# Optimization experiments

Measured on AMD Instinct MI355X. Metric: run time of the kernel, lower is better.

The kernel has to match this reference:

```python
import jax, jax.numpy as jnp
import numpy as np

N, E = 40000, 640000
DIN, HID, H = 512, 128, 4
C = HID  # per-head channels; H*C == 512 == DIN
BN_EPS = 1e-5


def setup_inputs() -> dict:
    key = jax.random.key(0)
    ks = jax.random.split(key, 32)
    sc = 0.05
    d = {}
    d["x"] = jax.random.normal(ks[0], (N, DIN), jnp.float32)
    d["edge_index"] = jax.random.randint(ks[1], (2, E), 0, N)
    i = 2
    for l in (1, 2, 3):
        d[f"W{l}"] = jax.random.normal(ks[i], (DIN, H * C), jnp.float32) * sc; i += 1
        d[f"as{l}"] = jax.random.normal(ks[i], (H, C), jnp.float32) * sc; i += 1
        d[f"ad{l}"] = jax.random.normal(ks[i], (H, C), jnp.float32) * sc; i += 1
        d[f"b{l}"] = jnp.zeros((H * C,), jnp.float32)
        d[f"g{l}"] = jnp.ones((H * C,), jnp.float32)
        d[f"be{l}"] = jnp.zeros((H * C,), jnp.float32)
    d["Wg1"] = jax.random.normal(ks[i], (H * C, HID), jnp.float32) * sc; i += 1
    d["bg1"] = jnp.zeros((HID,), jnp.float32)
    d["Wg2"] = jax.random.normal(ks[i], (HID, 1), jnp.float32) * sc; i += 1
    d["bg2"] = jnp.zeros((1,), jnp.float32)
    d["Wf1"] = jax.random.normal(ks[i], (H * C, HID), jnp.float32) * sc; i += 1
    d["bf1"] = jnp.zeros((HID,), jnp.float32)
    d["Wf2"] = jax.random.normal(ks[i], (HID, HID), jnp.float32) * sc; i += 1
    d["bf2"] = jnp.zeros((HID,), jnp.float32)
    d["Wp"] = jax.random.normal(ks[i], (HID + H * C, HID), jnp.float32) * sc; i += 1
    d["bp"] = jnp.zeros((HID,), jnp.float32)
    return d


def _gat(x, src, dst, W, a_s, a_d, b):
    # PyG GATConv (concat=True, negative_slope=0.2, self-loops already in src/dst)
    n = x.shape[0]
    h = (x @ W).reshape(n, H, C)                      # [N,H,C]
    es = jnp.einsum('nhc,hc->nh', h, a_s)             # alpha_src per node
    ed = jnp.einsum('nhc,hc->nh', h, a_d)             # alpha_dst per node
    e = jax.nn.leaky_relu(es[src] + ed[dst], 0.2)     # [Etot,H]
    m = jax.ops.segment_max(e, dst, num_segments=n)   # softmax over incoming edges
    ex = jnp.exp(e - m[dst])
    s = jax.ops.segment_sum(ex, dst, num_segments=n)
    w = ex / (s[dst] + 1e-16)                         # [Etot,H]
    out = jax.ops.segment_sum(w[:, :, None] * h[src], dst, num_segments=n)
    return out.reshape(n, H * C) + b


def _bn(x, g, b):
    mu = x.mean(0)
    var = x.var(0)
    return (x - mu) * jax.lax.rsqrt(var + BN_EPS) * g + b


def reference(x, edge_index,
              W1, as1, ad1, b1, g1, be1,
              W2, as2, ad2, b2, g2, be2,
              W3, as3, ad3, b3, g3, be3,
              Wg1, bg1, Wg2, bg2, Wf1, bf1, Wf2, bf2, Wp, bp):
    n = x.shape[0]
    loops = jnp.arange(n)
    src = jnp.concatenate([edge_index[0], loops])
    dst = jnp.concatenate([edge_index[1], loops])

    h = jax.nn.leaky_relu(_bn(_gat(x, src, dst, W1, as1, ad1, b1), g1, be1), 0.2)
    h_res = h
    h = jax.nn.leaky_relu(_bn(_gat(h, src, dst, W2, as2, ad2, b2), g2, be2), 0.2) + h_res
    h_res = h
    h = jax.nn.leaky_relu(_bn(_gat(h, src, dst, W3, as3, ad3, b3), g3, be3), 0.2) + h_res

    attn_scores = (jnp.tanh(h @ Wg1 + bg1) @ Wg2 + bg2)[:, 0]   # [N]
    attn_w = jax.nn.softmax(attn_scores)                        # softmax over all nodes
    feat = jax.nn.relu(h @ Wf1 + bf1) @ Wf2 + bf2               # [N,HID]
    gated = (attn_w[:, None] * feat).sum(0)                     # [HID]
    global_pooled = h.mean(0, keepdims=True)                    # batch=None -> one graph
    combined = jnp.concatenate([gated[None, :], global_pooled], axis=-1)  # [1,640]
    out = (combined @ Wp + bp)[0]                               # [HID]
    return out, attn_scores
```

## Files before the change

### kernel.cpp

```cpp
#include <hip/hip_runtime.h>
#include <math.h>

#define N_NODES 40000
#define M_PAD   40064
#define N_EDGES 640000
#define ETOT    (N_EDGES + N_NODES)
#define DINC    512
#define NHEAD   4
#define CHD     128
#define BN_EPS  1e-5f

typedef __attribute__((ext_vector_type(8))) short bf16x8;
typedef __attribute__((ext_vector_type(4))) float f32x4;

static __device__ __forceinline__ float lrelu(float x) { return x > 0.f ? x : 0.2f * x; }

static __device__ __forceinline__ unsigned short f2b(float f) {
    union { float f; unsigned int u; } v; v.f = f;
    unsigned int r = (v.u + 0x7fff + ((v.u >> 16) & 1)) >> 16;
    return (unsigned short)r;
}
static __device__ __forceinline__ float b2f(unsigned short b) {
    union { unsigned int u; float f; } v; v.u = ((unsigned int)b) << 16;
    return v.f;
}
static __device__ __forceinline__ float lo16(unsigned int u) {
    union { unsigned int u; float f; } v; v.u = u << 16; return v.f;
}
static __device__ __forceinline__ float hi16(unsigned int u) {
    union { unsigned int u; float f; } v; v.u = u & 0xffff0000u; return v.f;
}

static __device__ __forceinline__ void fma8(float* acc, uint4 hv, float wgt) {
    acc[0] += wgt * lo16(hv.x); acc[1] += wgt * hi16(hv.x);
    acc[2] += wgt * lo16(hv.y); acc[3] += wgt * hi16(hv.y);
    acc[4] += wgt * lo16(hv.z); acc[5] += wgt * hi16(hv.z);
    acc[6] += wgt * lo16(hv.w); acc[7] += wgt * hi16(hv.w);
}

#define GLDS16(g, l) __builtin_amdgcn_global_load_lds( \
    (__attribute__((address_space(1))) void*)(g),      \
    (__attribute__((address_space(3))) void*)(l), 16, 0, 0)

#define CVTX_BLK 10000
#define PREP_CVTW0 (CVTX_BLK + 72)
__global__ __launch_bounds__(256) void k_prep(const float4* __restrict__ xin,
                                              uint4* __restrict__ xb,
                                              uint4* __restrict__ curb,
                                              uint4* __restrict__ cnt4,
                                              const float* __restrict__ W1, unsigned short* __restrict__ T1,
                                              const float* __restrict__ W2, unsigned short* __restrict__ T2,
                                              const float* __restrict__ W3, unsigned short* __restrict__ T3,
                                              const float* __restrict__ Wg1, const float* __restrict__ Wf1,
                                              unsigned short* __restrict__ Wct) {
    int bid = blockIdx.x;
    int tid = threadIdx.x;
    if (bid < CVTX_BLK) {
        size_t i = (size_t)bid * 256 + tid;
        float4 a = xin[i * 2], b = xin[i * 2 + 1];
        uint4 o;
        o.x = (unsigned)f2b(a.x) | ((unsigned)f2b(a.y) << 16);
        o.y = (unsigned)f2b(a.z) | ((unsigned)f2b(a.w) << 16);
        o.z = (unsigned)f2b(b.x) | ((unsigned)f2b(b.y) << 16);
        o.w = (unsigned)f2b(b.z) | ((unsigned)f2b(b.w) << 16);
        xb[i] = o;
    } else if (bid < CVTX_BLK + 16) {
        int i = (bid - CVTX_BLK) * 256 + tid;
        xb[(size_t)N_NODES * DINC / 8 + i] = make_uint4(0, 0, 0, 0);
    } else if (bid < CVTX_BLK + 32) {
        int i = (bid - CVTX_BLK - 16) * 256 + tid;
        curb[(size_t)N_NODES * DINC / 8 + i] = make_uint4(0, 0, 0, 0);
    } else if (bid < PREP_CVTW0) {
        int i = (bid - CVTX_BLK - 32) * 256 + tid;
        if (i < N_NODES / 4) cnt4[i] = make_uint4(0, 0, 0, 0);
    } else {
        int idx = (bid - PREP_CVTW0) * 256 + tid;
        const float* W; unsigned short* T; int Nn;
        if (idx < 262144)            { W = W1; T = T1; Nn = 512; }
        else if (idx < 524288)       { W = W2; T = T2; Nn = 512; idx -= 262144; }
        else if (idx < 786432)       { W = W3; T = T3; Nn = 512; idx -= 524288; }
        else if (idx < 851968)       { W = Wg1; T = Wct; Nn = 128; idx -= 786432; }
        else                         { W = Wf1; T = Wct + 65536; Nn = 128; idx -= 851968; }
        int k = idx / Nn, n = idx % Nn;
        T[(size_t)n * 512 + k] = f2b(W[idx]);
    }
}

__global__ void k_degree(const int* __restrict__ ei, int* __restrict__ cnt) {
    int e = blockIdx.x * 256 + threadIdx.x;
    if (e < ETOT) {
        int dst = (e < N_EDGES) ? ei[N_EDGES + e] : (e - N_EDGES);
        atomicAdd(&cnt[dst], 1);
    }
}

__global__ __launch_bounds__(64) void k_scan1(const int* __restrict__ deg, int* __restrict__ bsum) {
    int lane = threadIdx.x;
    int v = deg[blockIdx.x * 64 + lane];
#pragma unroll
    for (int off = 32; off; off >>= 1) v += __shfl_xor(v, off);
    if (lane == 0) bsum[blockIdx.x] = v;
}

__global__ __launch_bounds__(64) void k_scan23(const int* __restrict__ deg, const int* __restrict__ bsum,
                                               int* __restrict__ rowptr, int* __restrict__ cnt) {
    int b = blockIdx.x, lane = threadIdx.x;
    int pre = 0;
    for (int i = lane; i < b; i += 64) pre += bsum[i];
#pragma unroll
    for (int off = 32; off; off >>= 1) pre += __shfl_xor(pre, off);
    int i = b * 64 + lane;
    int v = deg[i];
    int inc = v;
#pragma unroll
    for (int off = 1; off < 64; off <<= 1) {
        int t = __shfl_up(inc, off);
        if (lane >= off) inc += t;
    }
    rowptr[i] = pre + inc - v;
    cnt[i] = 0;
    if (b == 624 && lane == 63) rowptr[N_NODES] = ETOT;
}

__global__ void k_fill(const int* __restrict__ ei, const int* __restrict__ rowptr,
                       int* __restrict__ cnt, int* __restrict__ csr_src) {
    int e = blockIdx.x * 256 + threadIdx.x;
    if (e < ETOT) {
        int src, dst;
        if (e < N_EDGES) { src = ei[e]; dst = ei[N_EDGES + e]; }
        else             { src = e - N_EDGES; dst = src; }
        int pos = rowptr[dst] + atomicAdd(&cnt[dst], 1);
        csr_src[pos] = src;
    }
}

template<int CBF16, int EPI>
__global__ __launch_bounds__(256) void k_gemm_mfma(const unsigned short* __restrict__ A,
                                                   const unsigned short* __restrict__ Bt,
                                                   void* __restrict__ Cout,
                                                   int Nn, int K, int nbn,
                                                   const float* __restrict__ p1,
                                                   const float* __restrict__ p2,
                                                   float* __restrict__ p3,
                                                   float* __restrict__ p4,
                                                   const float* __restrict__ p5,
                                                   const float* __restrict__ p6) {
    __shared__ alignas(16) unsigned short As[128 * 64];
    __shared__ alignas(16) unsigned short Bs[128 * 64];
    const int tid  = threadIdx.x;
    const int wv   = tid >> 6;
    const int lane = tid & 63;
    const int bm = (blockIdx.x / nbn) * 128;
    const int bn = (blockIdx.x % nbn) * 128;
    const int wm = (wv >> 1) * 64;
    const int wn = (wv & 1) * 64;

    const int srow = lane >> 3;
    const int scol = (((lane & 7) ^ srow) * 8);
    const size_t a_base = (size_t)(bm + wv * 32 + srow) * K + scol;
    const size_t b_base = (size_t)(bn + wv * 32 + srow) * K + scol;

    f32x4 acc[4][4] = {};

    for (int k0 = 0; k0 < K; k0 += 64) {
#pragma unroll
        for (int q = 0; q < 4; ++q)
            GLDS16(A + a_base + (size_t)q * 8 * K + k0, &As[(wv * 32 + q * 8) * 64]);
#pragma unroll
        for (int q = 0; q < 4; ++q)
            GLDS16(Bt + b_base + (size_t)q * 8 * K + k0, &Bs[(wv * 32 + q * 8) * 64]);
        __syncthreads();

        const int r0 = lane & 15;
#pragma unroll
        for (int ks = 0; ks < 2; ++ks) {
            const int c = ks * 4 + (lane >> 4);
            bf16x8 af[4], bfr[4];
#pragma unroll
            for (int i = 0; i < 4; ++i) {
                int row = wm + i * 16 + r0;
                af[i] = *(const bf16x8*)&As[row * 64 + ((c ^ (row & 7)) * 8)];
            }
#pragma unroll
            for (int j = 0; j < 4; ++j) {
                int row = wn + j * 16 + r0;
                bfr[j] = *(const bf16x8*)&Bs[row * 64 + ((c ^ (row & 7)) * 8)];
            }
#pragma unroll
            for (int i = 0; i < 4; ++i)
#pragma unroll
                for (int j = 0; j < 4; ++j)
                    acc[i][j] = __builtin_amdgcn_mfma_f32_16x16x32_bf16(af[i], bfr[j], acc[i][j], 0, 0, 0);
        }
        __syncthreads();
    }

    const int crow0 = bm + wm + (lane >> 4) * 4;
    const int ccol  = bn + wn + (lane & 15);

    if (EPI != 2) {
#pragma unroll
        for (int i = 0; i < 4; ++i)
#pragma unroll
            for (int j = 0; j < 4; ++j)
#pragma unroll
                for (int r = 0; r < 4; ++r) {
                    size_t off = (size_t)(crow0 + i * 16 + r) * Nn + ccol + j * 16;
                    if (CBF16) ((unsigned short*)Cout)[off] = f2b(acc[i][j][r]);
                    else       ((float*)Cout)[off] = acc[i][j][r];
                }
    }

    if (EPI == 1) {
        const int head = bn >> 7;
        float asv[4], adv[4];
#pragma unroll
        for (int j = 0; j < 4; ++j) {
            int cc = head * CHD + wn + j * 16 + (lane & 15);
            asv[j] = p1[cc];
            adv[j] = p2[cc];
        }
        float* sE = (float*)As;
        sE[tid] = 0.f;
        __syncthreads();
#pragma unroll
        for (int i = 0; i < 4; ++i)
#pragma unroll
            for (int r = 0; r < 4; ++r) {
                float e = acc[i][0][r] * asv[0] + acc[i][1][r] * asv[1]
                        + acc[i][2][r] * asv[2] + acc[i][3][r] * asv[3];
                float d = acc[i][0][r] * adv[0] + acc[i][1][r] * adv[1]
                        + acc[i][2][r] * adv[2] + acc[i][3][r] * adv[3];
#pragma unroll
                for (int off = 8; off; off >>= 1) {
                    e += __shfl_xor(e, off);
                    d += __shfl_xor(d, off);
                }
                if ((lane & 15) == 0) {
                    int rloc = wm + i * 16 + (lane >> 4) * 4 + r;
                    atomicAdd(&sE[rloc], e);
                    atomicAdd(&sE[128 + rloc], d);
                }
            }
        __syncthreads();
        if (tid < 128) {
            p3[(size_t)(bm + tid) * NHEAD + head] = sE[tid];
            p4[(size_t)(bm + tid) * NHEAD + head] = sE[128 + tid];
        }
    }

    if (EPI == 2) {
        if (bn == 0) {
            float wgv[4], bgv[4];
#pragma unroll
            for (int j = 0; j < 4; ++j) {
                int cc = wn + j * 16 + (lane & 15);
                bgv[j] = p1[cc];
                wgv[j] = p2[cc];
            }
            float* sE = (float*)As;
            sE[tid] = 0.f;
            __syncthreads();
#pragma unroll
            for (int i = 0; i < 4; ++i)
#pragma unroll
                for (int r = 0; r < 4; ++r) {
                    float e = tanhf(acc[i][0][r] + bgv[0]) * wgv[0]
                            + tanhf(acc[i][1][r] + bgv[1]) * wgv[1]
                            + tanhf(acc[i][2][r] + bgv[2]) * wgv[2]
                            + tanhf(acc[i][3][r] + bgv[3]) * wgv[3];
#pragma unroll
                    for (int off = 8; off; off >>= 1) e += __shfl_xor(e, off);
                    if ((lane & 15) == 0)
                        atomicAdd(&sE[wm + i * 16 + (lane >> 4) * 4 + r], e);
                }
            __syncthreads();
            if (tid < 128) p3[bm + tid] = sE[tid] + p5[0];
        } else {
#pragma unroll
            for (int j = 0; j < 4; ++j) {
                int colF = wn + j * 16 + (lane & 15);
                float bv = p6[colF];
#pragma unroll
                for (int i = 0; i < 4; ++i)
#pragma unroll
                    for (int r = 0; r < 4; ++r)
                        p4[(size_t)(crow0 + i * 16 + r) * 128 + colF] =
                            fmaxf(acc[i][j][r] + bv, 0.f);
            }
        }
    }
}

__global__ __launch_bounds__(256) void k_wts(const float4* __restrict__ es4,
                                             const float4* __restrict__ ed4,
                                             const int* __restrict__ rowptr,
                                             const int* __restrict__ csr_src,
                                             uint2* __restrict__ wbuf2,
                                             float4* __restrict__ inv4,
                                             float* __restrict__ stats) {
    if (blockIdx.x == 0)
        for (int q = threadIdx.x; q < DINC * 2; q += 256) stats[q] = 0.f;
    int n = blockIdx.x * 4 + (threadIdx.x >> 6);
    int lane = threadIdx.x & 63;
    int start = rowptr[n], end = rowptr[n + 1];
    float4 edn = ed4[n];
    float4 sum = make_float4(0.f, 0.f, 0.f, 0.f);
    for (int j0 = start; j0 < end; j0 += 64) {
        int j = j0 + lane;
        if (j < end) {
            int s = csr_src[j];
            float4 e = es4[s];
            float4 ex;
            ex.x = __expf(lrelu(e.x + edn.x));
            ex.y = __expf(lrelu(e.y + edn.y));
            ex.z = __expf(lrelu(e.z + edn.z));
            ex.w = __expf(lrelu(e.w + edn.w));
            wbuf2[j] = make_uint2((unsigned)f2b(ex.x) | ((unsigned)f2b(ex.y) << 16),
                                  (unsigned)f2b(ex.z) | ((unsigned)f2b(ex.w) << 16));
            sum.x += ex.x; sum.y += ex.y; sum.z += ex.z; sum.w += ex.w;
        }
    }
#pragma unroll
    for (int off = 32; off; off >>= 1) {
        sum.x += __shfl_xor(sum.x, off);
        sum.y += __shfl_xor(sum.y, off);
        sum.z += __shfl_xor(sum.z, off);
        sum.w += __shfl_xor(sum.w, off);
    }
    if (lane == 0) {
        float4 iv;
        iv.x = 1.f / (sum.x + 1e-16f);
        iv.y = 1.f / (sum.y + 1e-16f);
        iv.z = 1.f / (sum.z + 1e-16f);
        iv.w = 1.f / (sum.w + 1e-16f);
        inv4[n] = iv;
    }
}

__global__ __launch_bounds__(256) void k_agg(const unsigned short* __restrict__ hb,
                                             const int* __restrict__ rowptr,
                                             const int* __restrict__ csr_src,
                                             const unsigned* __restrict__ wbufu,
                                             const float* __restrict__ invp,
                                             unsigned short* __restrict__ aggb) {
    __shared__ float part[4][512];
    const int n = blockIdx.x;
    const int tid = threadIdx.x;
    const int grp = tid >> 6;
    const int lane = tid & 63;
    const int head = lane >> 4;
    const int hh = head >> 1;
    const int start = rowptr[n], end = rowptr[n + 1];

    float acc[8] = {};
    int j = start + grp;
    int s_n = 0; unsigned wu_n = 0;
    if (j < end) { s_n = csr_src[j]; wu_n = wbufu[j * 2 + hh]; }
    while (j < end) {
        int s = s_n; unsigned wu = wu_n;
        int j2 = j + 4;
        if (j2 < end) { s_n = csr_src[j2]; wu_n = wbufu[j2 * 2 + hh]; }
        float wgt = (head & 1) ? hi16(wu) : lo16(wu);
        uint4 hv = *(const uint4*)&hb[(size_t)s * DINC + lane * 8];
        fma8(acc, hv, wgt);
        j = j2;
    }
    *(float4*)&part[grp][lane * 8]     = make_float4(acc[0], acc[1], acc[2], acc[3]);
    *(float4*)&part[grp][lane * 8 + 4] = make_float4(acc[4], acc[5], acc[6], acc[7]);
    __syncthreads();
    const int c = tid * 2;
    float v0 = part[0][c] + part[1][c] + part[2][c] + part[3][c];
    float v1 = part[0][c + 1] + part[1][c + 1] + part[2][c + 1] + part[3][c + 1];
    float iv = invp[(n << 2) + (c >> 7)];
    v0 *= iv; v1 *= iv;
    unsigned int o = (unsigned)f2b(v0) | ((unsigned)f2b(v1) << 16);
    *(unsigned int*)&aggb[(size_t)n * DINC + c] = o;
}

__global__ __launch_bounds__(256) void k_bn_stats(const unsigned short* __restrict__ aggb,
                                                  float* __restrict__ stats) {
    int tid = threadIdx.x;
    int row0 = blockIdx.x * 64;
    int c0 = tid * 2;
    float s0 = 0, q0 = 0, s1 = 0, q1 = 0;
    for (int r = row0; r < row0 + 64; ++r) {
        unsigned int hv = *(const unsigned int*)&aggb[(size_t)r * DINC + c0];
        float v0 = lo16(hv), v1 = hi16(hv);
        s0 += v0; q0 += v0 * v0;
        s1 += v1; q1 += v1 * v1;
    }
    atomicAdd(&stats[c0], s0);
    atomicAdd(&stats[c0 + 1], s1);
    atomicAdd(&stats[DINC + c0], q0);
    atomicAdd(&stats[DINC + c0 + 1], q1);
}

__global__ __launch_bounds__(256) void k_bn_act(const unsigned short* __restrict__ aggb,
                                                const float* __restrict__ stats,
                                                const float* __restrict__ g,
                                                const float* __restrict__ be,
                                                unsigned short* __restrict__ curb,
                                                int res) {
    size_t idx = (size_t)blockIdx.x * 256 + threadIdx.x;
    int c8 = ((int)(idx & 63)) * 8;
    uint4 v = *(const uint4*)&aggb[idx * 8];
    float xv[8] = { lo16(v.x), hi16(v.x), lo16(v.y), hi16(v.y),
                    lo16(v.z), hi16(v.z), lo16(v.w), hi16(v.w) };
#pragma unroll
    for (int q = 0; q < 8; ++q) {
        int c = c8 + q;
        float mu = stats[c] * (1.f / N_NODES);
        float var = stats[DINC + c] * (1.f / N_NODES) - mu * mu;
        float A = g[c] * rsqrtf(var + BN_EPS);
        float B = be[c] - mu * A;
        xv[q] = lrelu(xv[q] * A + B);
    }
    if (res) {
        uint4 r = *(const uint4*)&curb[idx * 8];
        xv[0] += lo16(r.x); xv[1] += hi16(r.x);
        xv[2] += lo16(r.y); xv[3] += hi16(r.y);
        xv[4] += lo16(r.z); xv[5] += hi16(r.z);
        xv[6] += lo16(r.w); xv[7] += hi16(r.w);
    }
    uint4 o;
    o.x = (unsigned)f2b(xv[0]) | ((unsigned)f2b(xv[1]) << 16);
    o.y = (unsigned)f2b(xv[2]) | ((unsigned)f2b(xv[3]) << 16);
    o.z = (unsigned)f2b(xv[4]) | ((unsigned)f2b(xv[5]) << 16);
    o.w = (unsigned)f2b(xv[6]) | ((unsigned)f2b(xv[7]) << 16);
    *(uint4*)&curb[idx * 8] = o;
}

__global__ __launch_bounds__(1024) void k_softmax(const float4* __restrict__ scores4,
                                                  const float* __restrict__ scores,
                                                  float* __restrict__ sm,
                                                  float* __restrict__ vbuf, float* __restrict__ pooled) {
    __shared__ float red[16];
    int tid = threadIdx.x, lane = tid & 63, wv = tid >> 6;
    if (tid < 128) vbuf[tid] = 0.f;
    if (tid < DINC) pooled[tid] = 0.f;
    float m = -1e30f;
    for (int i = tid; i < N_NODES / 4; i += 1024) {
        float4 s4 = scores4[i];
        m = fmaxf(fmaxf(fmaxf(m, s4.x), fmaxf(s4.y, s4.z)), s4.w);
    }
#pragma unroll
    for (int off = 32; off; off >>= 1) m = fmaxf(m, __shfl_xor(m, off));
    if (lane == 0) red[wv] = m;
    __syncthreads();
    float mall = red[0];
    for (int i = 1; i < 16; ++i) mall = fmaxf(mall, red[i]);
    __syncthreads();
    float s = 0.f;
    for (int i = tid; i < N_NODES / 4; i += 1024) {
        float4 s4 = scores4[i];
        s += __expf(s4.x - mall) + __expf(s4.y - mall) + __expf(s4.z - mall) + __expf(s4.w - mall);
    }
#pragma unroll
    for (int off = 32; off; off >>= 1) s += __shfl_xor(s, off);
    if (lane == 0) red[wv] = s;
    __syncthreads();
    if (tid == 0) {
        float tot = 0.f;
        for (int i = 0; i < 16; ++i) tot += red[i];
        sm[0] = mall; sm[1] = tot;
    }
}

__global__ __launch_bounds__(384) void k_vpool(const float* __restrict__ Fb,
                                               const unsigned short* __restrict__ hb,
                                               const float* __restrict__ scores,
                                               const float* __restrict__ sm,
                                               float* __restrict__ v,
                                               float* __restrict__ pooled) {
    int tid = threadIdx.x;
    int row0 = blockIdx.x * 64;
    float mall = sm[0];
    float invS = 1.f / sm[1];
    if (tid < 128) {
        float acc = 0.f;
        for (int r = row0; r < row0 + 64; ++r) {
            float w = __expf(scores[r] - mall) * invS;
            acc += w * Fb[(size_t)r * 128 + tid];
        }
        atomicAdd(&v[tid], acc);
    } else {
        int c = (tid - 128) * 2;
        float a0 = 0.f, a1 = 0.f;
        for (int r = row0; r < row0 + 64; ++r) {
            unsigned int hv = *(const unsigned int*)&hb[(size_t)r * DINC + c];
            a0 += lo16(hv); a1 += hi16(hv);
        }
        atomicAdd(&pooled[c], a0 * (1.f / N_NODES));
        atomicAdd(&pooled[c + 1], a1 * (1.f / N_NODES));
    }
}

__global__ __launch_bounds__(128) void k_final(const float* __restrict__ v,
                                               const float* __restrict__ pooled,
                                               const float* __restrict__ Wf2,
                                               const float* __restrict__ bf2,
                                               const float* __restrict__ Wp,
                                               const float* __restrict__ bp,
                                               float* __restrict__ out) {
    __shared__ float sg[128];
    int o = threadIdx.x;
    float g = bf2[o];
    for (int k = 0; k < 128; ++k) g += v[k] * Wf2[k * 128 + o];
    sg[o] = g;
    __syncthreads();
    float acc = bp[o];
    for (int c = 0; c < 128; ++c) acc += sg[c] * Wp[c * 128 + o];
    for (int j = 0; j < 512; ++j) acc += pooled[j] * Wp[(128 + j) * 128 + o];
    out[o] = acc;
}

extern "C" void kernel_launch(void* const* d_in, const int* in_sizes, int n_in,
                              void* d_out, int out_size, void* d_ws, size_t ws_size,
                              hipStream_t stream) {
    const float* x  = (const float*)d_in[0];
    const int*   ei = (const int*)d_in[1];
    const float* Wg1 = (const float*)d_in[20];
    const float* bg1 = (const float*)d_in[21];
    const float* Wg2 = (const float*)d_in[22];
    const float* bg2 = (const float*)d_in[23];
    const float* Wf1 = (const float*)d_in[24];
    const float* bf1 = (const float*)d_in[25];
    const float* Wf2 = (const float*)d_in[26];
    const float* bf2 = (const float*)d_in[27];
    const float* Wp  = (const float*)d_in[28];
    const float* bp  = (const float*)d_in[29];
    float* out = (float*)d_out;

    char* base = (char*)d_ws;
    size_t off = 0;
    auto take = [&](size_t nbytes) -> char* {
        char* p = base + off;
        off += (nbytes + 255) & ~(size_t)255;
        return p;
    };
    unsigned short* hb   = (unsigned short*)take((size_t)M_PAD * DINC * 2);
    unsigned short* curb = (unsigned short*)take((size_t)M_PAD * DINC * 2);
    unsigned short* xb   = (unsigned short*)take((size_t)M_PAD * DINC * 2);
    unsigned short* aggb = (unsigned short*)take((size_t)M_PAD * DINC * 2);
    float* Fb    = (float*)take((size_t)M_PAD * 128 * 4);
    float* es    = (float*)take((size_t)M_PAD * NHEAD * 4);
    float* ed    = (float*)take((size_t)M_PAD * NHEAD * 4);
    uint2* wbuf  = (uint2*)take((size_t)ETOT * 8);
    float* invp  = (float*)take((size_t)N_NODES * NHEAD * 4);
    int*   rowptr= (int*)take((size_t)(N_NODES + 1) * 4);
    int*   cnt   = (int*)take((size_t)N_NODES * 4);
    int*   csr   = (int*)take((size_t)ETOT * 4);
    int*   bsum  = (int*)take(625 * 4);
    float* stats = (float*)take(DINC * 2 * 4);
    float* sm    = (float*)take(2 * 4);
    float* vbuf  = (float*)take(128 * 4);
    float* pooled= (float*)take(DINC * 4);
    unsigned short* Wt1  = (unsigned short*)take((size_t)DINC * DINC * 2);
    unsigned short* Wt2  = (unsigned short*)take((size_t)DINC * DINC * 2);
    unsigned short* Wt3  = (unsigned short*)take((size_t)DINC * DINC * 2);
    unsigned short* Wct  = (unsigned short*)take((size_t)256 * DINC * 2);

    k_prep<<<PREP_CVTW0 + 3584, 256, 0, stream>>>((const float4*)x, (uint4*)xb,
                                                  (uint4*)curb, (uint4*)cnt,
                                                  (const float*)d_in[2], Wt1,
                                                  (const float*)d_in[8], Wt2,
                                                  (const float*)d_in[14], Wt3,
                                                  Wg1, Wf1, Wct);
    k_degree<<<(ETOT + 255) / 256, 256, 0, stream>>>(ei, cnt);
    k_scan1<<<625, 64, 0, stream>>>(cnt, bsum);
    k_scan23<<<625, 64, 0, stream>>>(cnt, bsum, rowptr, cnt);
    k_fill<<<(ETOT + 255) / 256, 256, 0, stream>>>(ei, rowptr, cnt, csr);

    const unsigned short* Wts[3] = {Wt1, Wt2, Wt3};
    const unsigned short* in = xb;
    for (int l = 0; l < 3; ++l) {
        const float* as_ = (const float*)d_in[2 + l * 6 + 1];
        const float* ad_ = (const float*)d_in[2 + l * 6 + 2];
        const float* g   = (const float*)d_in[2 + l * 6 + 4];
        const float* be  = (const float*)d_in[2 + l * 6 + 5];

        k_gemm_mfma<1, 1><<<(M_PAD / 128) * (DINC / 128), 256, 0, stream>>>(
            in, Wts[l], hb, DINC, DINC, DINC / 128, as_, ad_, es, ed, nullptr, nullptr);
        k_wts<<<N_NODES / 4, 256, 0, stream>>>((const float4*)es, (const float4*)ed, rowptr, csr,
                                               wbuf, (float4*)invp, stats);
        k_agg<<<N_NODES, 256, 0, stream>>>(hb, rowptr, csr, (const unsigned*)wbuf, invp, aggb);
        k_bn_stats<<<N_NODES / 64, 256, 0, stream>>>(aggb, stats);
        k_bn_act<<<(N_NODES * (DINC / 8)) / 256, 256, 0, stream>>>(aggb, stats, g, be, curb, l > 0 ? 1 : 0);
        in = curb;
    }

    float* scores = out + 128;
    k_gemm_mfma<0, 2><<<(M_PAD / 128) * 2, 256, 0, stream>>>(
        curb, Wct, nullptr, 256, DINC, 2, bg1, Wg2, scores, Fb, bg2, bf1);

    k_softmax<<<1, 1024, 0, stream>>>((const float4*)scores, scores, sm, vbuf, pooled);
    k_vpool<<<N_NODES / 64, 384, 0, stream>>>(Fb, curb, scores, sm, vbuf, pooled);
    k_final<<<1, 128, 0, stream>>>(vbuf, pooled, Wf2, bf2, Wp, bp, out);
}
```

Baseline: 836.2 us.

## Remap GEMM blocks per XCD, deepen gather prefetch, store FC features in bf16

Three independent changes. The GEMM block index is remapped so consecutive tiles are placed on the same XCD, aiming for better L2 reuse of A and B tiles on the chiplet design. The aggregation loop now software-pipelines the neighbour feature row load one iteration ahead, in addition to prefetching indices and weights, to hide gather latency. The gated-feature buffer Fb is written and read as bf16 instead of fp32, which halves its traffic but adds rounding error.

```diff
diff --git a/kernel.cpp b/kernel.cpp
--- a/kernel.cpp
+++ b/kernel.cpp
@@ -150,8 +150,13 @@
     const int tid  = threadIdx.x;
     const int wv   = tid >> 6;
     const int lane = tid & 63;
-    const int bm = (blockIdx.x / nbn) * 128;
-    const int bn = (blockIdx.x % nbn) * 128;
+    const int nwg  = gridDim.x;
+    const int orig = blockIdx.x;
+    const int qq = nwg >> 3, rr = nwg & 7;
+    const int xcd = orig & 7;
+    const int wgid = (xcd < rr ? xcd * (qq + 1) : rr * (qq + 1) + (xcd - rr) * qq) + (orig >> 3);
+    const int bm = (wgid / nbn) * 128;
+    const int bn = (wgid % nbn) * 128;
     const int wm = (wv >> 1) * 64;
     const int wn = (wv & 1) * 64;
 
@@ -277,6 +282,7 @@
             __syncthreads();
             if (tid < 128) p3[bm + tid] = sE[tid] + p5[0];
         } else {
+            unsigned short* Fb = (unsigned short*)p4;
 #pragma unroll
             for (int j = 0; j < 4; ++j) {
                 int colF = wn + j * 16 + (lane & 15);
@@ -285,8 +291,8 @@
                 for (int i = 0; i < 4; ++i)
 #pragma unroll
                     for (int r = 0; r < 4; ++r)
-                        p4[(size_t)(crow0 + i * 16 + r) * 128 + colF] =
-                            fmaxf(acc[i][j][r] + bv, 0.f);
+                        Fb[(size_t)(crow0 + i * 16 + r) * 128 + colF] =
+                            f2b(fmaxf(acc[i][j][r] + bv, 0.f));
             }
         }
     }
@@ -355,16 +361,27 @@
 
     float acc[8] = {};
     int j = start + grp;
-    int s_n = 0; unsigned wu_n = 0;
-    if (j < end) { s_n = csr_src[j]; wu_n = wbufu[j * 2 + hh]; }
+    int sA = 0; unsigned wA = 0;
+    uint4 hA = make_uint4(0, 0, 0, 0);
+    if (j < end) {
+        sA = csr_src[j]; wA = wbufu[j * 2 + hh];
+        hA = *(const uint4*)&hb[(size_t)sA * DINC + lane * 8];
+    }
+    int jB = j + 4;
+    int sB = 0; unsigned wB = 0;
+    if (jB < end) { sB = csr_src[jB]; wB = wbufu[jB * 2 + hh]; }
     while (j < end) {
-        int s = s_n; unsigned wu = wu_n;
-        int j2 = j + 4;
-        if (j2 < end) { s_n = csr_src[j2]; wu_n = wbufu[j2 * 2 + hh]; }
-        float wgt = (head & 1) ? hi16(wu) : lo16(wu);
-        uint4 hv = *(const uint4*)&hb[(size_t)s * DINC + lane * 8];
-        fma8(acc, hv, wgt);
-        j = j2;
+        uint4 hN = make_uint4(0, 0, 0, 0);
+        if (jB < end) hN = *(const uint4*)&hb[(size_t)sB * DINC + lane * 8];
+        int jC = jB + 4;
+        int sC = 0; unsigned wC = 0;
+        if (jC < end) { sC = csr_src[jC]; wC = wbufu[jC * 2 + hh]; }
+        float wgt = (head & 1) ? hi16(wA) : lo16(wA);
+        fma8(acc, hA, wgt);
+        j = jB; jB = jC;
+        wA = wB; wB = wC;
+        sB = sC;
+        hA = hN;
     }
     *(float4*)&part[grp][lane * 8]     = make_float4(acc[0], acc[1], acc[2], acc[3]);
     *(float4*)&part[grp][lane * 8 + 4] = make_float4(acc[4], acc[5], acc[6], acc[7]);
@@ -467,7 +484,7 @@
     }
 }
 
-__global__ __launch_bounds__(384) void k_vpool(const float* __restrict__ Fb,
+__global__ __launch_bounds__(384) void k_vpool(const unsigned short* __restrict__ Fb,
                                                const unsigned short* __restrict__ hb,
                                                const float* __restrict__ scores,
                                                const float* __restrict__ sm,
@@ -481,7 +498,7 @@
         float acc = 0.f;
         for (int r = row0; r < row0 + 64; ++r) {
             float w = __expf(scores[r] - mall) * invS;
-            acc += w * Fb[(size_t)r * 128 + tid];
+            acc += w * b2f(Fb[(size_t)r * 128 + tid]);
         }
         atomicAdd(&v[tid], acc);
     } else {
@@ -543,7 +560,7 @@
     unsigned short* curb = (unsigned short*)take((size_t)M_PAD * DINC * 2);
     unsigned short* xb   = (unsigned short*)take((size_t)M_PAD * DINC * 2);
     unsigned short* aggb = (unsigned short*)take((size_t)M_PAD * DINC * 2);
-    float* Fb    = (float*)take((size_t)M_PAD * 128 * 4);
+    unsigned short* Fb   = (unsigned short*)take((size_t)M_PAD * 128 * 2);
     float* es    = (float*)take((size_t)M_PAD * NHEAD * 4);
     float* ed    = (float*)take((size_t)M_PAD * NHEAD * 4);
     uint2* wbuf  = (uint2*)take((size_t)ETOT * 8);
@@ -592,7 +609,7 @@
 
     float* scores = out + 128;
     k_gemm_mfma<0, 2><<<(M_PAD / 128) * 2, 256, 0, stream>>>(
-        curb, Wct, nullptr, 256, DINC, 2, bg1, Wg2, scores, Fb, bg2, bf1);
+        curb, Wct, nullptr, 256, DINC, 2, bg1, Wg2, scores, (float*)Fb, bg2, bf1);
 
     k_softmax<<<1, 1024, 0, stream>>>((const float4*)scores, scores, sm, vbuf, pooled);
     k_vpool<<<N_NODES / 64, 384, 0, stream>>>(Fb, curb, scores, sm, vbuf, pooled);
```

Measured after the change: 850.0 us. Within noise of the previous version (+1.6%).
